# Kernel tuning notes

Measured on AMD Instinct MI355X. Metric: run time of the kernel, lower is better.

## Reference

```python
import jax, jax.numpy as jnp
import numpy as np

HEADS = 8
B, N, DIM = 8, 1024, 128  # n must be a perfect square (H=W=32)
LN_EPS = 1e-5


def _region_means(xg):
    """Four-quadrant region means per position via integral image.
    xg: [b,H,W,d] -> [b,H,W,4,d]. For position (h,w) the torch code pools:
      r1 = x[:, :h+1, :w+1], r2 = x[:, :h+1, w:], r3 = x[:, h:, :w+1], r4 = x[:, h:, w:]
    """
    b, H, W, d = xg.shape
    # padded 2D prefix sum: P[:, i, j] = sum over rows<i, cols<j
    P = jnp.pad(jnp.cumsum(jnp.cumsum(xg, axis=1), axis=2),
                ((0, 0), (1, 0), (1, 0), (0, 0)))
    r1 = P[:, 1:, 1:]                                              # sum x[:h+1,:w+1]
    r2 = P[:, 1:, -1:] - P[:, 1:, :-1]                             # sum x[:h+1, w:]
    r3 = P[:, -1:, 1:] - P[:, :-1, 1:]                             # sum x[h:, :w+1]
    r4 = P[:, -1:, -1:] - P[:, :-1, -1:] - P[:, -1:, :-1] + P[:, :-1, :-1]
    ah = jnp.arange(H, dtype=xg.dtype)
    aw = jnp.arange(W, dtype=xg.dtype)
    hp1 = (ah + 1.0)[:, None]   # h+1
    wp1 = (aw + 1.0)[None, :]   # w+1
    hr = (H - ah)[:, None]      # H-h
    wr = (W - aw)[None, :]      # W-w
    c1 = (hp1 * wp1)[None, :, :, None]
    c2 = (hp1 * wr)[None, :, :, None]
    c3 = (hr * wp1)[None, :, :, None]
    c4 = (hr * wr)[None, :, :, None]
    return jnp.stack([r1 / c1, r2 / c2, r3 / c3, r4 / c4], axis=3)


def setup_inputs() -> dict:
    key = jax.random.key(0)
    ks = jax.random.split(key, 10)
    s = 0.02
    return {
        "x": jax.random.normal(ks[0], (B, N, DIM), jnp.float32),
        "ln_g": jnp.ones((DIM,), jnp.float32),
        "ln_b": jnp.zeros((DIM,), jnp.float32),
        "Wqkv": jax.random.normal(ks[1], (DIM, 3 * HEADS * DIM), jnp.float32) * s,
        "bqkv": jax.random.normal(ks[2], (3 * HEADS * DIM,), jnp.float32) * s,
        "Wq": jax.random.normal(ks[3], (DIM, DIM), jnp.float32) * s,
        "Wk": jax.random.normal(ks[4], (DIM, DIM), jnp.float32) * s,
        "Wv": jax.random.normal(ks[5], (DIM, DIM), jnp.float32) * s,
        "Wo": jax.random.normal(ks[6], (DIM, DIM), jnp.float32) * s,
        "bo": jax.random.normal(ks[7], (DIM,), jnp.float32) * s,
        "Wout": jax.random.normal(ks[8], (HEADS * DIM, DIM), jnp.float32) * s,
        "bout": jax.random.normal(ks[9], (DIM,), jnp.float32) * s,
    }


def reference(x, ln_g, ln_b, Wqkv, bqkv, Wq, Wk, Wv, Wo, bo, Wout, bout):
    b, n, dim = x.shape
    H = W = int(n ** 0.5)
    # LayerNorm
    mu = jnp.mean(x, axis=-1, keepdims=True)
    var = jnp.mean(jnp.square(x - mu), axis=-1, keepdims=True)
    xn = (x - mu) * jax.lax.rsqrt(var + LN_EPS) * ln_g + ln_b
    # qkv projection; only q is actually used downstream (k,v chunks are dead)
    qkv = xn @ Wqkv + bqkv
    q = qkv[..., : HEADS * dim].reshape(b, n, HEADS, dim).transpose(0, 2, 1, 3)  # [b,h,n,d]
    # region features, identical across heads -> keep unbroadcast [b,n,4,d]
    regions = _region_means(xn.reshape(b, H, W, dim)).reshape(b, n, 4, dim)
    # RegionAggregator
    qh = q @ Wq                                   # [b,h,n,d]
    k = jnp.einsum('bnrd,de->bnre', regions, Wk)  # [b,n,4,d]
    v = jnp.einsum('bnrd,de->bnre', regions, Wv)
    scale = (dim // HEADS) ** -0.5
    attn = jax.nn.softmax(jnp.einsum('bhnd,bnrd->bhnr', qh, k) * scale, axis=-1)
    agg = jnp.einsum('bhnr,bnrd->bhnd', attn, v)
    out = agg @ Wo + bo                           # [b,h,n,d]
    out = out.transpose(0, 2, 1, 3).reshape(b, n, HEADS * dim)
    return out @ Wout + bout
```

## Files before the change

### kernel.cpp

```cpp
#include <hip/hip_runtime.h>
#include <hip/hip_bf16.h>
#include <stdint.h>

#define HEADS 8
#define NN 1024
#define DIM 128
#define HW 32
#define LN_EPS 1e-5f

typedef __hip_bfloat16 bf16;
typedef __bf16 bf16x8 __attribute__((ext_vector_type(8)));
typedef float floatx4 __attribute__((ext_vector_type(4)));

__device__ __forceinline__ float b2f(bf16 v){ return __bfloat162float(v); }
__device__ __forceinline__ bf16 f2b(float v){ return __float2bfloat16(v); }

__device__ __forceinline__ float ldin(const void* p, size_t i, int f){
    return f ? ((const float*)p)[i] : b2f(((const bf16*)p)[i]);
}
__device__ __forceinline__ float4 ldin4(const void* p, size_t i, int f){
    if (f) return *reinterpret_cast<const float4*>((const float*)p + i);
    ushort4 u = *reinterpret_cast<const ushort4*>((const bf16*)p + i);
    float4 r;
    r.x = b2f(*(bf16*)&u.x); r.y = b2f(*(bf16*)&u.y);
    r.z = b2f(*(bf16*)&u.z); r.w = b2f(*(bf16*)&u.w);
    return r;
}
__device__ __forceinline__ int dtf(const void* g){
    return (((const uint32_t*)g)[0] == 0x3F800000u) ? 1 : 0;
}

__global__ __launch_bounds__(256) void ln_kernel(const void* __restrict__ x,
                                                 const void* __restrict__ g,
                                                 const void* __restrict__ bta,
                                                 bf16* __restrict__ xn){
    int f = dtf(g);
    int row = blockIdx.x*4 + (threadIdx.x >> 6);
    int lane = threadIdx.x & 63;
    size_t base = (size_t)row*DIM;
    float v0 = ldin(x, base+lane,    f);
    float v1 = ldin(x, base+lane+64, f);
    float s = v0+v1, ss = v0*v0+v1*v1;
    for (int o=32;o;o>>=1){ s += __shfl_xor(s,o,64); ss += __shfl_xor(ss,o,64); }
    float mu = s * (1.0f/DIM);
    float var = ss * (1.0f/DIM) - mu*mu;
    float rs = rsqrtf(var + LN_EPS);
    float y0 = (v0-mu)*rs*ldin(g,lane,f)    + ldin(bta,lane,f);
    float y1 = (v1-mu)*rs*ldin(g,lane+64,f) + ldin(bta,lane+64,f);
    xn[base+lane]    = f2b(y0);
    xn[base+lane+64] = f2b(y1);
}

__global__ __launch_bounds__(128) void rowscan_kernel(const bf16* __restrict__ xn,
                                                      float* __restrict__ P){
    int b = blockIdx.x >> 5, h = blockIdx.x & 31, c = threadIdx.x;
    const bf16* xr = xn + ((size_t)(b*NN + h*HW))*DIM + c;
    float* Pr = P + ((size_t)(b*NN + h*HW))*DIM + c;
    float run = 0.f;
    for (int w=0; w<HW; w++){ run += b2f(xr[(size_t)w*DIM]); Pr[(size_t)w*DIM] = run; }
}

__global__ __launch_bounds__(128) void colscan_kernel(float* __restrict__ P){
    int b = blockIdx.x >> 5, w = blockIdx.x & 31, c = threadIdx.x;
    float* Pc = P + ((size_t)(b*NN + w))*DIM + c;
    float run = 0.f;
    for (int h=0; h<HW; h++){
        size_t o = (size_t)h*HW*DIM;
        run += Pc[o]; Pc[o] = run;
    }
}

__global__ __launch_bounds__(256) void prep_kernel(const void* __restrict__ Wqkv,
                                                   const void* __restrict__ bqkv,
                                                   const void* __restrict__ Wq,
                                                   const void* __restrict__ Wk,
                                                   const void* __restrict__ Wv,
                                                   const void* __restrict__ Wo,
                                                   const void* __restrict__ bo,
                                                   const void* __restrict__ Wout,
                                                   const void* __restrict__ ln_g,
                                                   bf16* __restrict__ WhT,
                                                   bf16* __restrict__ WhoT,
                                                   bf16* __restrict__ WkvT,
                                                   float* __restrict__ bq,
                                                   float* __restrict__ bfin_part){
    __shared__ float S1[128][132];
    __shared__ float S2[8][132];
    int f = dtf(ln_g);
    int t = threadIdx.x;
    int blk = blockIdx.x;
    if (blk < 128){
        int h = blk >> 4, dc = blk & 15;
#pragma unroll
        for (int i=0;i<16;i++){
            int idx4 = (t + i*256)*4;
            int k = idx4 >> 7, e = idx4 & 127;
            *reinterpret_cast<float4*>(&S1[k][e]) = ldin4(Wq, idx4, f);
        }
        {
            int idx4 = t*4;
            int dl = idx4 >> 7, k = idx4 & 127;
            *reinterpret_cast<float4*>(&S2[dl][k]) =
                ldin4(Wqkv, (size_t)(dc*8+dl)*3072 + h*128 + k, f);
        }
        __syncthreads();
        int d = t & 7;
        int e0 = (t >> 3) * 4;
        float acc[4] = {0.f,0.f,0.f,0.f};
        for (int k=0;k<128;k++){
            float a = S2[d][k];
            float4 wv = *reinterpret_cast<const float4*>(&S1[k][e0]);
            acc[0] += a*wv.x; acc[1] += a*wv.y; acc[2] += a*wv.z; acc[3] += a*wv.w;
        }
#pragma unroll
        for (int i=0;i<4;i++)
            WhT[(size_t)(h*128 + e0 + i)*128 + dc*8 + d] = f2b(acc[i]);
    } else if (blk < 256){
        int h = (blk-128) >> 4, dc = (blk-128) & 15;
#pragma unroll
        for (int i=0;i<16;i++){
            int idx4 = (t + i*256)*4;
            int k = idx4 >> 7, e = idx4 & 127;
            *reinterpret_cast<float4*>(&S1[k][e]) =
                ldin4(Wout, (size_t)(h*128 + k)*128 + e, f);
        }
        {
            int idx4 = t*4;
            int dl = idx4 >> 7, k = idx4 & 127;
            *reinterpret_cast<float4*>(&S2[dl][k]) =
                ldin4(Wo, (size_t)(dc*8+dl)*128 + k, f);
        }
        __syncthreads();
        int d = t & 7;
        int e0 = (t >> 3) * 4;
        float acc[4] = {0.f,0.f,0.f,0.f};
        for (int k=0;k<128;k++){
            float a = S2[d][k];
            float4 wv = *reinterpret_cast<const float4*>(&S1[k][e0]);
            acc[0] += a*wv.x; acc[1] += a*wv.y; acc[2] += a*wv.z; acc[3] += a*wv.w;
        }
#pragma unroll
        for (int i=0;i<4;i++)
            WhoT[(size_t)(e0 + i)*1024 + h*128 + dc*8 + d] = f2b(acc[i]);
    } else {
        int sub = blk - 256;
        if (sub < 8){
            int h = sub;
            int e = t & 127, kh = t >> 7;
            float s = 0.f;
            for (int k=kh*64; k<kh*64+64; k++)
                s += ldin(bqkv, h*128 + k, f) * ldin(Wq, (size_t)k*128 + e, f);
            S1[kh][e] = s;
            __syncthreads();
            if (t < 128) bq[h*128 + t] = S1[0][t] + S1[1][t];
        } else if (sub < 16){
            int h = sub - 8;
            if (t < 128) S2[0][t] = ldin(bo, t, f);
            __syncthreads();
            int e = t & 127, half = t >> 7;
            float s = 0.f;
            for (int k = half*64; k < half*64 + 64; k++)
                s += S2[0][k] * ldin(Wout, (size_t)(h*128 + k)*128 + e, f);
            S1[half][e] = s;
            __syncthreads();
            if (t < 128) bfin_part[h*128 + t] = S1[0][t] + S1[1][t];
        } else {
            const void* W = (sub == 16) ? Wk : Wv;
            int base = (sub == 16) ? 0 : 128;
#pragma unroll
            for (int i=0;i<16;i++){
                int idx4 = (t + i*256)*4;
                int d = idx4 >> 7, e = idx4 & 127;
                *reinterpret_cast<float4*>(&S1[d][e]) = ldin4(W, idx4, f);
            }
            __syncthreads();
            for (int i=0;i<64;i++){
                int idx = t + i*256; int e = idx >> 7, d = idx & 127;
                WkvT[(size_t)(base + e)*128 + d] = f2b(S1[d][e]);
            }
        }
    }
}

__global__ __launch_bounds__(256) void gemm_mfma_kernel(const bf16* __restrict__ A,
                                                        const bf16* __restrict__ BT,
                                                        const float* __restrict__ bias,
                                                        bf16* __restrict__ C,
                                                        int M, int N, int K){
    __shared__ __align__(16) bf16 As[64][136];
    __shared__ __align__(16) bf16 Bs[64][136];
    int t = threadIdx.x;
    int w = t >> 6, lane = t & 63;
    int r = lane & 15, q = lane >> 4;
    int m0 = blockIdx.y * 64, n0 = blockIdx.x * 64;
    floatx4 acc[4];
#pragma unroll
    for (int nt=0;nt<4;nt++) acc[nt] = (floatx4){0.f,0.f,0.f,0.f};

    for (int kt = 0; kt < K; kt += 128){
#pragma unroll
        for (int c=0;c<4;c++){
            int id = t + c*256;
            int row = id >> 4, c8 = id & 15;
            *reinterpret_cast<uint4*>(&As[row][c8*8]) =
                *reinterpret_cast<const uint4*>(&A[(size_t)(m0+row)*K + kt + c8*8]);
            *reinterpret_cast<uint4*>(&Bs[row][c8*8]) =
                *reinterpret_cast<const uint4*>(&BT[(size_t)(n0+row)*K + kt + c8*8]);
        }
        __syncthreads();
#pragma unroll
        for (int kc=0;kc<4;kc++){
            bf16x8 a = *reinterpret_cast<const bf16x8*>(&As[w*16 + r][kc*32 + q*8]);
#pragma unroll
            for (int nt=0;nt<4;nt++){
                bf16x8 b = *reinterpret_cast<const bf16x8*>(&Bs[nt*16 + r][kc*32 + q*8]);
                acc[nt] = __builtin_amdgcn_mfma_f32_16x16x32_bf16(a, b, acc[nt], 0, 0, 0);
            }
        }
        __syncthreads();
    }
#pragma unroll
    for (int nt=0;nt<4;nt++){
#pragma unroll
        for (int i=0;i<4;i++){
            int row = m0 + w*16 + q*4 + i;
            int col = n0 + nt*16 + r;
            C[(size_t)row*N + col] = f2b(acc[nt][i] + (bias ? bias[col] : 0.f));
        }
    }
}

__global__ __launch_bounds__(256) void kv_kernel(const float* __restrict__ P,
                                                 const bf16* __restrict__ WkvT,
                                                 bf16* __restrict__ kvmat){
    __shared__ __align__(16) bf16 As[64][136];
    __shared__ __align__(16) bf16 Bs[128][136];
    int t = threadIdx.x;
    int bn0 = blockIdx.x * 16;
    {
        int bn_local = t >> 4;
        int c0 = (t & 15) * 8;
        int bn = bn0 + bn_local;
        int b = bn >> 10, n = bn & 1023;
        int hh = n >> 5, ww = n & 31;
        const float* Pb = P + (size_t)b*NN*DIM;
        auto ld8 = [&](int h, int w, float* o){
            if (h==0 || w==0){
#pragma unroll
                for (int j=0;j<8;j++) o[j] = 0.f;
                return;
            }
            const float* p = Pb + ((size_t)((h-1)*HW + (w-1)))*DIM + c0;
            float4 u = *reinterpret_cast<const float4*>(p);
            float4 v = *reinterpret_cast<const float4*>(p+4);
            o[0]=u.x;o[1]=u.y;o[2]=u.z;o[3]=u.w;o[4]=v.x;o[5]=v.y;o[6]=v.z;o[7]=v.w;
        };
        float f_h1 = (float)(hh+1), f_w1 = (float)(ww+1);
        float f_hr = (float)(HW-hh), f_wr = (float)(HW-ww);
        float a0[8], a1[8];
        ld8(hh+1, ww+1, a0);
#pragma unroll
        for (int j=0;j<8;j++) As[bn_local*4 + 0][c0+j] = f2b(a0[j] / (f_h1*f_w1));
        ld8(hh+1, HW, a0); ld8(hh+1, ww, a1);
#pragma unroll
        for (int j=0;j<8;j++) As[bn_local*4 + 1][c0+j] = f2b((a0[j]-a1[j]) / (f_h1*f_wr));
        ld8(HW, ww+1, a0); ld8(hh, ww+1, a1);
#pragma unroll
        for (int j=0;j<8;j++) As[bn_local*4 + 2][c0+j] = f2b((a0[j]-a1[j]) / (f_hr*f_w1));
        float a2[8], a3[8];
        ld8(HW, HW, a0); ld8(hh, HW, a1); ld8(HW, ww, a2); ld8(hh, ww, a3);
#pragma unroll
        for (int j=0;j<8;j++)
            As[bn_local*4 + 3][c0+j] = f2b((a0[j]-a1[j]-a2[j]+a3[j]) / (f_hr*f_wr));
    }
    int w = t >> 6, lane = t & 63;
    int r = lane & 15, q = lane >> 4;
    floatx4 acc[16];
#pragma unroll
    for (int i=0;i<16;i++) acc[i] = (floatx4){0.f,0.f,0.f,0.f};
    for (int half=0; half<2; half++){
        __syncthreads();
#pragma unroll
        for (int i=0;i<8;i++){
            int id = t + i*256;
            int row = id >> 4, c8 = id & 15;
            *reinterpret_cast<uint4*>(&Bs[row][c8*8]) =
                *reinterpret_cast<const uint4*>(&WkvT[(size_t)(half*128 + row)*128 + c8*8]);
        }
        __syncthreads();
#pragma unroll
        for (int kc=0;kc<4;kc++){
            bf16x8 a = *reinterpret_cast<const bf16x8*>(&As[w*16 + r][kc*32 + q*8]);
#pragma unroll
            for (int nt=0;nt<8;nt++){
                bf16x8 b = *reinterpret_cast<const bf16x8*>(&Bs[nt*16 + r][kc*32 + q*8]);
                acc[half*8+nt] = __builtin_amdgcn_mfma_f32_16x16x32_bf16(a, b, acc[half*8+nt], 0, 0, 0);
            }
        }
    }
#pragma unroll
    for (int half=0; half<2; half++)
#pragma unroll
    for (int nt=0;nt<8;nt++){
#pragma unroll
        for (int i=0;i<4;i++){
            int row = bn0*4 + w*16 + q*4 + i;
            int col = half*128 + nt*16 + r;
            kvmat[(size_t)row*256 + col] = f2b(acc[half*8+nt][i]);
        }
    }
}

__global__ __launch_bounds__(512) void probs_kernel(const bf16* __restrict__ qh,
                                                    const bf16* __restrict__ kvmat,
                                                    float* __restrict__ probs){
    __shared__ float kS[4][DIM];
    int bn = blockIdx.x, t = threadIdx.x;
    if (t < 128){
        int rr = t >> 5, c4 = (t & 31)*4;
#pragma unroll
        for (int j=0;j<4;j++)
            kS[rr][c4+j] = b2f(kvmat[(size_t)(bn*4 + rr)*256 + c4 + j]);
    }
    __syncthreads();
    int h = t >> 6, lane = t & 63;
    float q0 = b2f(qh[(size_t)bn*1024 + h*128 + lane]);
    float q1 = b2f(qh[(size_t)bn*1024 + h*128 + 64 + lane]);
    float l0 = q0*kS[0][lane] + q1*kS[0][lane+64];
    float l1 = q0*kS[1][lane] + q1*kS[1][lane+64];
    float l2 = q0*kS[2][lane] + q1*kS[2][lane+64];
    float l3 = q0*kS[3][lane] + q1*kS[3][lane+64];
    for (int o=32;o;o>>=1){
        l0 += __shfl_xor(l0,o,64); l1 += __shfl_xor(l1,o,64);
        l2 += __shfl_xor(l2,o,64); l3 += __shfl_xor(l3,o,64);
    }
    l0 *= 0.25f; l1 *= 0.25f; l2 *= 0.25f; l3 *= 0.25f;
    float m = fmaxf(fmaxf(l0,l1),fmaxf(l2,l3));
    float e0 = __expf(l0-m), e1=__expf(l1-m), e2=__expf(l2-m), e3=__expf(l3-m);
    float inv = 1.0f/(e0+e1+e2+e3);
    float pv = (lane==0) ? e0 : (lane==1) ? e1 : (lane==2) ? e2 : e3;
    if (lane < 4) probs[(size_t)bn*32 + h*4 + lane] = pv * inv;
}

__global__ __launch_bounds__(256) void out_kernel(const float* __restrict__ probs,
                                                  const bf16* __restrict__ kvmat,
                                                  const bf16* __restrict__ WhoT,
                                                  const float* __restrict__ bfin_part,
                                                  const void* __restrict__ bout,
                                                  const void* __restrict__ ln_g,
                                                  void* __restrict__ out){
    __shared__ __align__(16) bf16 v_lds[4][32][136];
    __shared__ __align__(16) bf16 Bs[128][136];
    __shared__ __align__(16) float p_lds[32][36];
    int f = dtf(ln_g);
    int t = threadIdx.x;
    int bn0 = blockIdx.x * 32;
#pragma unroll
    for (int i=0;i<8;i++){
        int id = t + i*256;
        int c8 = id & 15, row = (id >> 4) & 31, rg = id >> 9;
        *reinterpret_cast<uint4*>(&v_lds[rg][row][c8*8]) =
            *reinterpret_cast<const uint4*>(&kvmat[(size_t)((bn0+row)*4 + rg)*256 + 128 + c8*8]);
    }
#pragma unroll
    for (int i=0;i<4;i++){
        int id = t + i*256;
        int row = id >> 5, col = id & 31;
        p_lds[row][col] = probs[(size_t)bn0*32 + id];
    }
    int w = t >> 6, lane = t & 63;
    int r = lane & 15, q = lane >> 4;
    int mh = w & 1, nh = w >> 1;
    int myrow = mh*16 + r;
    floatx4 acc[4];
#pragma unroll
    for (int nt=0;nt<4;nt++) acc[nt] = (floatx4){0.f,0.f,0.f,0.f};

    for (int h=0; h<8; h++){
        __syncthreads();
#pragma unroll
        for (int i=0;i<8;i++){
            int id = t + i*256;
            int row = id >> 4, c8 = id & 15;
            *reinterpret_cast<uint4*>(&Bs[row][c8*8]) =
                *reinterpret_cast<const uint4*>(&WhoT[(size_t)row*1024 + h*128 + c8*8]);
        }
        __syncthreads();
        float4 pv = *reinterpret_cast<const float4*>(&p_lds[myrow][h*4]);
#pragma unroll
        for (int kc=0;kc<4;kc++){
            int c = kc*32 + q*8;
            bf16x8 v0 = *reinterpret_cast<const bf16x8*>(&v_lds[0][myrow][c]);
            bf16x8 v1 = *reinterpret_cast<const bf16x8*>(&v_lds[1][myrow][c]);
            bf16x8 v2 = *reinterpret_cast<const bf16x8*>(&v_lds[2][myrow][c]);
            bf16x8 v3 = *reinterpret_cast<const bf16x8*>(&v_lds[3][myrow][c]);
            bf16x8 a;
#pragma unroll
            for (int j=0;j<8;j++){
                float s = pv.x*(float)v0[j] + pv.y*(float)v1[j]
                        + pv.z*(float)v2[j] + pv.w*(float)v3[j];
                a[j] = (__bf16)s;
            }
#pragma unroll
            for (int nt=0;nt<4;nt++){
                bf16x8 b = *reinterpret_cast<const bf16x8*>(&Bs[nh*64 + nt*16 + r][kc*32 + q*8]);
                acc[nt] = __builtin_amdgcn_mfma_f32_16x16x32_bf16(a, b, acc[nt], 0, 0, 0);
            }
        }
    }
#pragma unroll
    for (int nt=0;nt<4;nt++){
        int col = nh*64 + nt*16 + r;
        float bias = ldin(bout, col, f);
#pragma unroll
        for (int h=0;h<8;h++) bias += bfin_part[h*128 + col];
#pragma unroll
        for (int i=0;i<4;i++){
            int row = bn0 + mh*16 + q*4 + i;
            float v = acc[nt][i] + bias;
            if (f) ((float*)out)[(size_t)row*DIM + col] = v;
            else   ((bf16*)out)[(size_t)row*DIM + col] = f2b(v);
        }
    }
}

extern "C" void kernel_launch(void* const* d_in, const int* in_sizes, int n_in,
                              void* d_out, int out_size, void* d_ws, size_t ws_size,
                              hipStream_t stream){
    const void* x    = d_in[0];
    const void* ln_g = d_in[1];
    const void* ln_b = d_in[2];
    const void* Wqkv = d_in[3];
    const void* bqkv = d_in[4];
    const void* Wq   = d_in[5];
    const void* Wk   = d_in[6];
    const void* Wv   = d_in[7];
    const void* Wo   = d_in[8];
    const void* bo   = d_in[9];
    const void* Wout = d_in[10];
    const void* bout = d_in[11];

    char* ws = (char*)d_ws;
    size_t off = 0;
    auto alloc = [&](size_t bytes)->char*{
        char* p = ws + off; off += (bytes + 255) & ~size_t(255); return p;
    };
    bf16*  WhT   = (bf16*)alloc((size_t)1024*128*2);
    bf16*  WkvT  = (bf16*)alloc((size_t)256*128*2);
    bf16*  WhoT  = (bf16*)alloc((size_t)128*1024*2);
    float* bq    = (float*)alloc(1024*4);
    float* bfin_part = (float*)alloc(8*128*4);
    float* P     = (float*)alloc((size_t)8*NN*DIM*4);
    bf16*  xn    = (bf16*)alloc((size_t)8192*128*2);
    bf16*  qh    = (bf16*)alloc((size_t)8192*1024*2);
    bf16*  kvmat = (bf16*)alloc((size_t)32768*256*2);
    float* probs = (float*)alloc((size_t)8192*32*4);

    prep_kernel<<<274, 256, 0, stream>>>(Wqkv, bqkv, Wq, Wk, Wv, Wo, bo, Wout,
                                         ln_g, WhT, WhoT, WkvT, bq, bfin_part);
    ln_kernel<<<2048, 256, 0, stream>>>(x, ln_g, ln_b, xn);
    rowscan_kernel<<<256, 128, 0, stream>>>(xn, P);
    colscan_kernel<<<256, 128, 0, stream>>>(P);
    gemm_mfma_kernel<<<dim3(16, 128), 256, 0, stream>>>(xn, WhT, bq, qh, 8192, 1024, 128);
    kv_kernel<<<512, 256, 0, stream>>>(P, WkvT, kvmat);
    probs_kernel<<<8192, 512, 0, stream>>>(qh, kvmat, probs);
    out_kernel<<<256, 256, 0, stream>>>(probs, kvmat, WhoT, bfin_part, bout, ln_g, d_out);
}
```

Baseline: 169.6 us.

## Fuse region key projection with attention-probability computation in one kernel

The separate probs kernel is merged into the kv kernel. K is kept in shared memory instead of being written to global memory, and the logits are computed with MFMA against a qh tile staged in LDS. Only V is written out, which halves the intermediate buffer and removes one launch plus the K round trip. The cost is higher LDS use per block (about 52KB, from aliasing a shared pool), which may reduce occupancy. Most MFMA output lanes are also discarded when extracting the diagonal logits.

```diff
diff --git a/kernel.cpp b/kernel.cpp
--- a/kernel.cpp
+++ b/kernel.cpp
@@ -230,11 +230,18 @@
     }
 }
 
-__global__ __launch_bounds__(256) void kv_kernel(const float* __restrict__ P,
-                                                 const bf16* __restrict__ WkvT,
-                                                 bf16* __restrict__ kvmat){
-    __shared__ __align__(16) bf16 As[64][136];
-    __shared__ __align__(16) bf16 Bs[128][136];
+__global__ __launch_bounds__(256) void kvprobs_kernel(const float* __restrict__ P,
+                                                      const bf16* __restrict__ WkvT,
+                                                      const bf16* __restrict__ qh,
+                                                      bf16* __restrict__ vmat,
+                                                      float* __restrict__ probs){
+    __shared__ __align__(16) char pool[52480];
+    bf16 (*As)[136] = reinterpret_cast<bf16(*)[136]>(pool);
+    bf16 (*Bs)[136] = reinterpret_cast<bf16(*)[136]>(pool + 17408);
+    bf16 (*kS)[16][136] = reinterpret_cast<bf16(*)[16][136]>(pool);
+    bf16 (*qhS)[1032]   = reinterpret_cast<bf16(*)[1032]>(pool + 17408);
+    float* logits       = reinterpret_cast<float*>(pool + 50432);
+
     int t = threadIdx.x;
     int bn0 = blockIdx.x * 16;
     {
@@ -299,51 +306,65 @@
         }
     }
 #pragma unroll
-    for (int half=0; half<2; half++)
-#pragma unroll
     for (int nt=0;nt<8;nt++){
 #pragma unroll
         for (int i=0;i<4;i++){
             int row = bn0*4 + w*16 + q*4 + i;
-            int col = half*128 + nt*16 + r;
-            kvmat[(size_t)row*256 + col] = f2b(acc[half*8+nt][i]);
-        }
-    }
-}
-
-__global__ __launch_bounds__(512) void probs_kernel(const bf16* __restrict__ qh,
-                                                    const bf16* __restrict__ kvmat,
-                                                    float* __restrict__ probs){
-    __shared__ float kS[4][DIM];
-    int bn = blockIdx.x, t = threadIdx.x;
+            int col = nt*16 + r;
+            vmat[(size_t)row*128 + col] = f2b(acc[8+nt][i]);
+        }
+    }
+    __syncthreads();
+#pragma unroll
+    for (int nt=0;nt<8;nt++){
+#pragma unroll
+        for (int i=0;i<4;i++){
+            int rowg = w*16 + q*4 + i;
+            kS[rowg & 3][rowg >> 2][nt*16 + r] = f2b(acc[nt][i]);
+        }
+    }
+#pragma unroll
+    for (int i=0;i<8;i++){
+        int id = t + i*256;
+        int row = id >> 7, c8 = id & 127;
+        *reinterpret_cast<uint4*>(&qhS[row][c8*8]) =
+            *reinterpret_cast<const uint4*>(&qh[(size_t)(bn0+row)*1024 + c8*8]);
+    }
+    __syncthreads();
+#pragma unroll
+    for (int h2=0; h2<2; h2++){
+        int h = w*2 + h2;
+#pragma unroll
+        for (int rg=0; rg<4; rg++){
+            floatx4 s = (floatx4){0.f,0.f,0.f,0.f};
+#pragma unroll
+            for (int kc=0;kc<4;kc++){
+                bf16x8 a = *reinterpret_cast<const bf16x8*>(&qhS[r][h*128 + kc*32 + q*8]);
+                bf16x8 b = *reinterpret_cast<const bf16x8*>(&kS[rg][r][kc*32 + q*8]);
+                s = __builtin_amdgcn_mfma_f32_16x16x32_bf16(a, b, s, 0, 0, 0);
+            }
+            if ((r >> 2) == q){
+                int i = r & 3;
+                float d = (i==0)?s[0]:(i==1)?s[1]:(i==2)?s[2]:s[3];
+                logits[(r*8 + h)*4 + rg] = d;
+            }
+        }
+    }
+    __syncthreads();
     if (t < 128){
-        int rr = t >> 5, c4 = (t & 31)*4;
-#pragma unroll
-        for (int j=0;j<4;j++)
-            kS[rr][c4+j] = b2f(kvmat[(size_t)(bn*4 + rr)*256 + c4 + j]);
-    }
-    __syncthreads();
-    int h = t >> 6, lane = t & 63;
-    float q0 = b2f(qh[(size_t)bn*1024 + h*128 + lane]);
-    float q1 = b2f(qh[(size_t)bn*1024 + h*128 + 64 + lane]);
-    float l0 = q0*kS[0][lane] + q1*kS[0][lane+64];
-    float l1 = q0*kS[1][lane] + q1*kS[1][lane+64];
-    float l2 = q0*kS[2][lane] + q1*kS[2][lane+64];
-    float l3 = q0*kS[3][lane] + q1*kS[3][lane+64];
-    for (int o=32;o;o>>=1){
-        l0 += __shfl_xor(l0,o,64); l1 += __shfl_xor(l1,o,64);
-        l2 += __shfl_xor(l2,o,64); l3 += __shfl_xor(l3,o,64);
-    }
-    l0 *= 0.25f; l1 *= 0.25f; l2 *= 0.25f; l3 *= 0.25f;
-    float m = fmaxf(fmaxf(l0,l1),fmaxf(l2,l3));
-    float e0 = __expf(l0-m), e1=__expf(l1-m), e2=__expf(l2-m), e3=__expf(l3-m);
-    float inv = 1.0f/(e0+e1+e2+e3);
-    float pv = (lane==0) ? e0 : (lane==1) ? e1 : (lane==2) ? e2 : e3;
-    if (lane < 4) probs[(size_t)bn*32 + h*4 + lane] = pv * inv;
+        int bn = t >> 3, h = t & 7;
+        const float* L = &logits[(bn*8 + h)*4];
+        float l0 = L[0]*0.25f, l1 = L[1]*0.25f, l2 = L[2]*0.25f, l3 = L[3]*0.25f;
+        float m = fmaxf(fmaxf(l0,l1),fmaxf(l2,l3));
+        float e0 = __expf(l0-m), e1=__expf(l1-m), e2=__expf(l2-m), e3=__expf(l3-m);
+        float inv = 1.0f/(e0+e1+e2+e3);
+        float4 pv = {e0*inv, e1*inv, e2*inv, e3*inv};
+        *reinterpret_cast<float4*>(&probs[(size_t)(bn0+bn)*32 + h*4]) = pv;
+    }
 }
 
 __global__ __launch_bounds__(256) void out_kernel(const float* __restrict__ probs,
-                                                  const bf16* __restrict__ kvmat,
+                                                  const bf16* __restrict__ vmat,
                                                   const bf16* __restrict__ WhoT,
                                                   const float* __restrict__ bfin_part,
                                                   const void* __restrict__ bout,
@@ -360,7 +381,7 @@
         int id = t + i*256;
         int c8 = id & 15, row = (id >> 4) & 31, rg = id >> 9;
         *reinterpret_cast<uint4*>(&v_lds[rg][row][c8*8]) =
-            *reinterpret_cast<const uint4*>(&kvmat[(size_t)((bn0+row)*4 + rg)*256 + 128 + c8*8]);
+            *reinterpret_cast<const uint4*>(&vmat[(size_t)((bn0+row)*4 + rg)*128 + c8*8]);
     }
 #pragma unroll
     for (int i=0;i<4;i++){
@@ -453,7 +474,7 @@
     float* P     = (float*)alloc((size_t)8*NN*DIM*4);
     bf16*  xn    = (bf16*)alloc((size_t)8192*128*2);
     bf16*  qh    = (bf16*)alloc((size_t)8192*1024*2);
-    bf16*  kvmat = (bf16*)alloc((size_t)32768*256*2);
+    bf16*  vmat  = (bf16*)alloc((size_t)32768*128*2);
     float* probs = (float*)alloc((size_t)8192*32*4);
 
     prep_kernel<<<274, 256, 0, stream>>>(Wqkv, bqkv, Wq, Wk, Wv, Wo, bo, Wout,
@@ -462,7 +483,6 @@
     rowscan_kernel<<<256, 128, 0, stream>>>(xn, P);
     colscan_kernel<<<256, 128, 0, stream>>>(P);
     gemm_mfma_kernel<<<dim3(16, 128), 256, 0, stream>>>(xn, WhT, bq, qh, 8192, 1024, 128);
-    kv_kernel<<<512, 256, 0, stream>>>(P, WkvT, kvmat);
-    probs_kernel<<<8192, 512, 0, stream>>>(qh, kvmat, probs);
-    out_kernel<<<256, 256, 0, stream>>>(probs, kvmat, WhoT, bfin_part, bout, ln_g, d_out);
-}
+    kvprobs_kernel<<<512, 256, 0, stream>>>(P, WkvT, qh, vmat, probs);
+    out_kernel<<<256, 256, 0, stream>>>(probs, vmat, WhoT, bfin_part, bout, ln_g, d_out);
+}
```

Measured after the change: 151.0 us, median of 2. -11.0%, faster.
